# Kernel optimization log

Measured on AMD Instinct MI355X. Metric: run time of the kernel, lower is better.

Reference implementation:

```python
import jax, jax.numpy as jnp
import numpy as np

B, IN, H, CTX = 16384, 1024, 1024, 2048


def setup_inputs() -> dict:
    key = jax.random.key(0)
    ks = jax.random.split(key, 20)
    stdv = 1.0 / np.sqrt(H)
    u = lambda k, shape: jax.random.uniform(k, shape, jnp.float32, -stdv, stdv)
    inp = {
        "y": jax.random.normal(ks[0], (B, IN), jnp.float32),
        "ctx": jax.random.normal(ks[1], (B, CTX), jnp.float32),
        "c0": jax.random.normal(ks[2], (B, H), jnp.float32),
        "h0": jax.random.normal(ks[3], (B, H), jnp.float32),
        # Concatenated gate weights in order (i, f, o, c), matching the
        # per-gate matrices Wi..Wc, Ui..Uc, Ci..Cc of the original module.
        "W": u(ks[4], (4 * H, IN)),   # input projections
        "U": u(ks[5], (4 * H, H)),    # hidden projections
        "C": u(ks[6], (4 * H, CTX)),  # context projections
        "b": u(ks[7], (4 * H,)),      # gate biases
    }
    return inp


def reference(y, ctx, c0, h0, W, U, C, b):
    # One fused GEMM per input stream instead of 12 small ones; same math.
    gates = y @ W.T + h0 @ U.T + ctx @ C.T + b  # [B, 4H]
    gi, gf, go, gc = jnp.split(gates, 4, axis=-1)
    i = jax.nn.sigmoid(gi)
    f = jax.nn.sigmoid(gf)
    o = jax.nn.sigmoid(go)
    c_hat = jnp.tanh(gc)
    c = i * c_hat + f * c0
    h = o * jnp.tanh(c)
    return (c, h)
```

## Files before the change

### kernel.cpp

```cpp
#include <hip/hip_runtime.h>
#include <hip/hip_bf16.h>
#include <stdint.h>

typedef __attribute__((ext_vector_type(8))) short short8;
typedef __attribute__((ext_vector_type(8))) unsigned short ushort8;
typedef __attribute__((ext_vector_type(4))) float f32x4;
typedef __attribute__((ext_vector_type(8))) __bf16 bf16x8;

#define GAS __attribute__((address_space(1)))
#define LAS __attribute__((address_space(3)))

static constexpr int Bn = 16384;
static constexpr int Hn = 1024;
static constexpr int KT = 4096;
static constexpr int BM = 256;
static constexpr int NT = KT / 64;

#define SBAR()   __builtin_amdgcn_s_barrier()
#define VMCNT(n) asm volatile("s_waitcnt vmcnt(" #n ")" ::: "memory")

__device__ __forceinline__ unsigned short f2bf(float f) {
  unsigned u = __builtin_bit_cast(unsigned, f);
  u = (u + 0x7FFFu + ((u >> 16) & 1u)) >> 16;
  return (unsigned short)u;
}

__device__ __forceinline__ float fast_sigm(float x) {
  return __builtin_amdgcn_rcpf(1.f + __expf(-x));
}
__device__ __forceinline__ float fast_tanh(float x) {
  return 1.f - 2.f * __builtin_amdgcn_rcpf(__expf(2.f * x) + 1.f);
}

__global__ __launch_bounds__(256) void cvt_concat_k(
    const float* __restrict__ s0, const float* __restrict__ s1,
    const float* __restrict__ s2, unsigned short* __restrict__ dst,
    long long n8) {
  long long stride = (long long)gridDim.x * blockDim.x;
  for (long long g = (long long)blockIdx.x * blockDim.x + threadIdx.x; g < n8;
       g += stride) {
    long long row = g >> 9;
    int cg = (int)(g & 511) << 3;
    const float* src;
    if (cg < 1024)      src = s0 + row * 1024 + cg;
    else if (cg < 2048) src = s1 + row * 1024 + (cg - 1024);
    else                src = s2 + row * 2048 + (cg - 2048);
    float4 f0 = *(const float4*)src;
    float4 f1 = *(const float4*)(src + 4);
    ushort8 o;
    o[0] = f2bf(f0.x); o[1] = f2bf(f0.y); o[2] = f2bf(f0.z); o[3] = f2bf(f0.w);
    o[4] = f2bf(f1.x); o[5] = f2bf(f1.y); o[6] = f2bf(f1.z); o[7] = f2bf(f1.w);
    *(ushort8*)(dst + (g << 3)) = o;
  }
}

__global__ __launch_bounds__(512, 2) void lstm_gemm(
    const unsigned short* __restrict__ X, const unsigned short* __restrict__ Wc,
    const float* __restrict__ bias, const float* __restrict__ c0,
    float* __restrict__ out_c, float* __restrict__ out_h) {
  extern __shared__ char smem[];

  int bid = blockIdx.x;
  int swz = (bid & 7) * 128 + (bid >> 3);
  int mblk = swz >> 4, cblk = swz & 15;
  int brow0 = mblk * BM;
  int hcol0 = cblk * 64;

  int tid = threadIdx.x;
  int lane = tid & 63, wid = tid >> 6;
  int wr = wid >> 2, wc = wid & 3;

  const char* Xc = (const char*)X;
  const char* Wcc = (const char*)Wc;

  int rr = tid >> 3;
  uint32_t cbyte = (uint32_t)(((tid & 7) * 16) ^ ((rr & 7) << 4));
  uint32_t aoff[2][2], boff[2][2];
#pragma unroll
  for (int half = 0; half < 2; ++half) {
#pragma unroll
    for (int j = 0; j < 2; ++j) {
      int r = half * 128 + j * 64 + rr;
      aoff[half][j] = (uint32_t)(brow0 + r) * (KT * 2) + cbyte;
      int w = ((r >> 4) & 3) * 1024 + hcol0 + ((r >> 6) << 4) + (r & 15);
      boff[half][j] = (uint32_t)w * (KT * 2) + cbyte;
    }
  }

  auto stage_half = [&](int isB, int half, int tt) {
    int ts = tt < NT ? tt : NT - 1;
    int bufs = tt & 1;
#pragma unroll
    for (int j = 0; j < 2; ++j) {
      uint32_t off = (isB ? boff[half][j] : aoff[half][j]) + (uint32_t)ts * 128u;
      const char* src = (isB ? Wcc : Xc) + off;
      char* dst = smem + bufs * 65536 + isB * 32768 + half * 16384 + j * 8192 +
                  wid * 1024;
      __builtin_amdgcn_global_load_lds((const GAS unsigned int*)src,
                                       (LAS unsigned int*)dst, 16, 0, 0);
    }
  };

  int kg = (lane >> 4) << 4;
  int sw = (lane & 7) << 4;
  int koff0 = (0 + kg) ^ sw;
  int koff1 = (64 + kg) ^ sw;
  int fr = lane & 15;

  f32x4 acc[8][4] = {};
  short8 bfr[4][2];

  stage_half(1, 0, 0);
  stage_half(1, 1, 0);
  stage_half(0, 0, 0);
  stage_half(0, 1, 0);
  stage_half(1, 0, 1);
  stage_half(1, 1, 1);
  stage_half(0, 0, 1);
  VMCNT(8);
  SBAR();

  for (int t = 0; t < NT; ++t) {
    int p = t & 1;
#pragma unroll
    for (int q = 0; q < 4; ++q) {
      if (q == 0) {
        int bb = p * 65536 + 32768 + (wc * 64 + fr) * 128;
#pragma unroll
        for (int n = 0; n < 4; ++n) {
          bfr[n][0] = *(const short8*)(smem + bb + n * 2048 + koff0);
          bfr[n][1] = *(const short8*)(smem + bb + n * 2048 + koff1);
        }
      }
      int ab = p * 65536 + ((2 * q + wr) * 32 + fr) * 128;
      short8 a0k0 = *(const short8*)(smem + ab + koff0);
      short8 a0k1 = *(const short8*)(smem + ab + koff1);
      short8 a1k0 = *(const short8*)(smem + ab + 2048 + koff0);
      short8 a1k1 = *(const short8*)(smem + ab + 2048 + koff1);

      if (q == 0)      stage_half(0, 1, t + 1);
      else if (q == 1) stage_half(1, 0, t + 2);
      else if (q == 2) stage_half(1, 1, t + 2);
      else             stage_half(0, 0, t + 2);

      SBAR();
      __builtin_amdgcn_s_setprio(1);
#pragma unroll
      for (int n = 0; n < 4; ++n) {
        acc[2 * q][n] = __builtin_amdgcn_mfma_f32_16x16x32_bf16(
            __builtin_bit_cast(bf16x8, a0k0), __builtin_bit_cast(bf16x8, bfr[n][0]),
            acc[2 * q][n], 0, 0, 0);
        acc[2 * q][n] = __builtin_amdgcn_mfma_f32_16x16x32_bf16(
            __builtin_bit_cast(bf16x8, a0k1), __builtin_bit_cast(bf16x8, bfr[n][1]),
            acc[2 * q][n], 0, 0, 0);
        acc[2 * q + 1][n] = __builtin_amdgcn_mfma_f32_16x16x32_bf16(
            __builtin_bit_cast(bf16x8, a1k0), __builtin_bit_cast(bf16x8, bfr[n][0]),
            acc[2 * q + 1][n], 0, 0, 0);
        acc[2 * q + 1][n] = __builtin_amdgcn_mfma_f32_16x16x32_bf16(
            __builtin_bit_cast(bf16x8, a1k1), __builtin_bit_cast(bf16x8, bfr[n][1]),
            acc[2 * q + 1][n], 0, 0, 0);
      }
      __builtin_amdgcn_s_setprio(0);

      if (q == 1) { VMCNT(10); }
      else if (q == 3) { VMCNT(8); }
      SBAR();
    }
  }

  int col = hcol0 + wc * 16 + fr;
  float bi = bias[col], bf_ = bias[1024 + col];
  float bo = bias[2048 + col], bc = bias[3072 + col];
#pragma unroll
  for (int m = 0; m < 8; ++m) {
    int row0 = brow0 + (2 * (m >> 1) + wr) * 32 + (m & 1) * 16 + ((lane >> 4) << 2);
#pragma unroll
    for (int j = 0; j < 4; ++j) {
      size_t idx = (size_t)(row0 + j) * 1024 + col;
      float i_ = fast_sigm(acc[m][0][j] + bi);
      float f_ = fast_sigm(acc[m][1][j] + bf_);
      float o_ = fast_sigm(acc[m][2][j] + bo);
      float ch = fast_tanh(acc[m][3][j] + bc);
      float cn = i_ * ch + f_ * c0[idx];
      out_c[idx] = cn;
      out_h[idx] = o_ * fast_tanh(cn);
    }
  }
}

__global__ __launch_bounds__(256) void lstm_naive(
    const float* __restrict__ y, const float* __restrict__ ctx,
    const float* __restrict__ c0, const float* __restrict__ h0,
    const float* __restrict__ W, const float* __restrict__ U,
    const float* __restrict__ C, const float* __restrict__ b,
    float* __restrict__ out_c, float* __restrict__ out_h) {
  size_t t = (size_t)blockIdx.x * blockDim.x + threadIdx.x;
  if (t >= (size_t)Bn * Hn) return;
  int row = (int)(t >> 10), col = (int)(t & 1023);
  float g[4];
#pragma unroll
  for (int gg = 0; gg < 4; ++gg) {
    int wrow = gg * 1024 + col;
    float s = b[wrow];
    const float* yr = y + (size_t)row * 1024;
    const float* Wr = W + (size_t)wrow * 1024;
    for (int k = 0; k < 1024; ++k) s += yr[k] * Wr[k];
    const float* hr = h0 + (size_t)row * 1024;
    const float* Ur = U + (size_t)wrow * 1024;
    for (int k = 0; k < 1024; ++k) s += hr[k] * Ur[k];
    const float* cr = ctx + (size_t)row * 2048;
    const float* Cr = C + (size_t)wrow * 2048;
    for (int k = 0; k < 2048; ++k) s += cr[k] * Cr[k];
    g[gg] = s;
  }
  float i_ = fast_sigm(g[0]), f_ = fast_sigm(g[1]);
  float o_ = fast_sigm(g[2]), ch = fast_tanh(g[3]);
  float cn = i_ * ch + f_ * c0[t];
  out_c[t] = cn;
  out_h[t] = o_ * fast_tanh(cn);
}

extern "C" void kernel_launch(void* const* d_in, const int* in_sizes, int n_in,
                              void* d_out, int out_size, void* d_ws, size_t ws_size,
                              hipStream_t stream) {
  const float* y   = (const float*)d_in[0];
  const float* ctx = (const float*)d_in[1];
  const float* c0  = (const float*)d_in[2];
  const float* h0  = (const float*)d_in[3];
  const float* W   = (const float*)d_in[4];
  const float* U   = (const float*)d_in[5];
  const float* C   = (const float*)d_in[6];
  const float* b   = (const float*)d_in[7];
  float* out = (float*)d_out;
  float* out_c = out;
  float* out_h = out + (size_t)Bn * Hn;

  const size_t needX = (size_t)Bn * KT * 2;
  const size_t needW = (size_t)(4 * Hn) * KT * 2;

  if (ws_size >= needX + needW) {
    unsigned short* Xb = (unsigned short*)d_ws;
    unsigned short* Wb = (unsigned short*)((char*)d_ws + needX);
    cvt_concat_k<<<2048, 256, 0, stream>>>(y, h0, ctx, Xb, (long long)Bn * 512);
    cvt_concat_k<<<2048, 256, 0, stream>>>(W, U, C, Wb, (long long)(4 * Hn) * 512);
    (void)hipFuncSetAttribute((const void*)lstm_gemm,
                              hipFuncAttributeMaxDynamicSharedMemorySize, 131072);
    lstm_gemm<<<1024, 512, 131072, stream>>>(Xb, Wb, b, c0, out_c, out_h);
  } else {
    lstm_naive<<<(Bn * Hn + 255) / 256, 256, 0, stream>>>(y, ctx, c0, h0, W, U, C,
                                                          b, out_c, out_h);
  }
}
```

Baseline: 557.2 us.

## Software-pipeline LDS fragment loads one phase ahead of MFMAs

Restructures the main GEMM loop so each phase loads the next phase's A fragments (and, at phase boundaries, the next tile's B k0 fragments) into double-buffered registers before running the current MFMAs. The loop is unrolled by two tiles so buffer indices are compile-time, and the vmcnt waits are moved and retuned. The aim is to hide LDS read latency behind matrix math. In exchange it uses more VGPRs and depends on correct wait and barrier placement for the prefetched buffers.

```diff
diff --git a/kernel.cpp b/kernel.cpp
--- a/kernel.cpp
+++ b/kernel.cpp
@@ -108,7 +108,9 @@
   int fr = lane & 15;
 
   f32x4 acc[8][4] = {};
-  short8 bfr[4][2];
+  short8 areg[2][4];
+  short8 bk0[2][4];
+  short8 bk1[4];
 
   stage_half(1, 0, 0);
   stage_half(1, 1, 0);
@@ -119,54 +121,85 @@
   stage_half(0, 0, 1);
   VMCNT(8);
   SBAR();
-
-  for (int t = 0; t < NT; ++t) {
-    int p = t & 1;
-#pragma unroll
-    for (int q = 0; q < 4; ++q) {
-      if (q == 0) {
-        int bb = p * 65536 + 32768 + (wc * 64 + fr) * 128;
-#pragma unroll
-        for (int n = 0; n < 4; ++n) {
-          bfr[n][0] = *(const short8*)(smem + bb + n * 2048 + koff0);
-          bfr[n][1] = *(const short8*)(smem + bb + n * 2048 + koff1);
-        }
-      }
-      int ab = p * 65536 + ((2 * q + wr) * 32 + fr) * 128;
-      short8 a0k0 = *(const short8*)(smem + ab + koff0);
-      short8 a0k1 = *(const short8*)(smem + ab + koff1);
-      short8 a1k0 = *(const short8*)(smem + ab + 2048 + koff0);
-      short8 a1k1 = *(const short8*)(smem + ab + 2048 + koff1);
-
-      if (q == 0)      stage_half(0, 1, t + 1);
-      else if (q == 1) stage_half(1, 0, t + 2);
-      else if (q == 2) stage_half(1, 1, t + 2);
-      else             stage_half(0, 0, t + 2);
-
-      SBAR();
-      __builtin_amdgcn_s_setprio(1);
-#pragma unroll
-      for (int n = 0; n < 4; ++n) {
-        acc[2 * q][n] = __builtin_amdgcn_mfma_f32_16x16x32_bf16(
-            __builtin_bit_cast(bf16x8, a0k0), __builtin_bit_cast(bf16x8, bfr[n][0]),
-            acc[2 * q][n], 0, 0, 0);
-        acc[2 * q][n] = __builtin_amdgcn_mfma_f32_16x16x32_bf16(
-            __builtin_bit_cast(bf16x8, a0k1), __builtin_bit_cast(bf16x8, bfr[n][1]),
-            acc[2 * q][n], 0, 0, 0);
-        acc[2 * q + 1][n] = __builtin_amdgcn_mfma_f32_16x16x32_bf16(
-            __builtin_bit_cast(bf16x8, a1k0), __builtin_bit_cast(bf16x8, bfr[n][0]),
-            acc[2 * q + 1][n], 0, 0, 0);
-        acc[2 * q + 1][n] = __builtin_amdgcn_mfma_f32_16x16x32_bf16(
-            __builtin_bit_cast(bf16x8, a1k1), __builtin_bit_cast(bf16x8, bfr[n][1]),
-            acc[2 * q + 1][n], 0, 0, 0);
-      }
-      __builtin_amdgcn_s_setprio(0);
-
-      if (q == 1) { VMCNT(10); }
-      else if (q == 3) { VMCNT(8); }
-      SBAR();
-    }
-  }
+  {
+    int bb = 32768 + (wc * 64 + fr) * 128;
+#pragma unroll
+    for (int n = 0; n < 4; ++n)
+      bk0[0][n] = *(const short8*)(smem + bb + n * 2048 + koff0);
+    int ab = (wr * 32 + fr) * 128;
+    areg[0][0] = *(const short8*)(smem + ab + koff0);
+    areg[0][1] = *(const short8*)(smem + ab + koff1);
+    areg[0][2] = *(const short8*)(smem + ab + 2048 + koff0);
+    areg[0][3] = *(const short8*)(smem + ab + 2048 + koff1);
+  }
+
+#define PHASE(Q_, P_, T_)                                                     \
+  {                                                                           \
+    constexpr int Q = (Q_);                                                   \
+    constexpr int P = (P_);                                                   \
+    const int t_ = (T_);                                                      \
+                                                     \
+    if (Q == 0)      stage_half(0, 1, t_ + 1);      \
+    else if (Q == 1) stage_half(1, 0, t_ + 2);      \
+    else if (Q == 2) stage_half(1, 1, t_ + 2);      \
+    else             stage_half(0, 0, t_ + 2);      \
+    if (Q == 0) { VMCNT(8); }                                                 \
+    if (Q == 2) { VMCNT(6); }                                                 \
+                                                \
+    if (Q < 3) {                                                              \
+      int ab = P * 65536 + ((2 * (Q + 1) + wr) * 32 + fr) * 128;              \
+      areg[(Q + 1) & 1][0] = *(const short8*)(smem + ab + koff0);             \
+      areg[(Q + 1) & 1][1] = *(const short8*)(smem + ab + koff1);             \
+      areg[(Q + 1) & 1][2] = *(const short8*)(smem + ab + 2048 + koff0);      \
+      areg[(Q + 1) & 1][3] = *(const short8*)(smem + ab + 2048 + koff1);      \
+    } else {                                                                  \
+      int ab = (P ^ 1) * 65536 + (wr * 32 + fr) * 128;                        \
+      areg[0][0] = *(const short8*)(smem + ab + koff0);                       \
+      areg[0][1] = *(const short8*)(smem + ab + koff1);                       \
+      areg[0][2] = *(const short8*)(smem + ab + 2048 + koff0);                \
+      areg[0][3] = *(const short8*)(smem + ab + 2048 + koff1);                \
+      int bb = (P ^ 1) * 65536 + 32768 + (wc * 64 + fr) * 128;                \
+      _Pragma("unroll")                                                       \
+      for (int n = 0; n < 4; ++n)                                             \
+        bk0[P ^ 1][n] = *(const short8*)(smem + bb + n * 2048 + koff0);       \
+    }                                                                         \
+    if (Q == 0) {                                                             \
+      int bb = P * 65536 + 32768 + (wc * 64 + fr) * 128;                      \
+      _Pragma("unroll")                                                       \
+      for (int n = 0; n < 4; ++n)                                             \
+        bk1[n] = *(const short8*)(smem + bb + n * 2048 + koff1);              \
+    }                                                                         \
+    SBAR();                                                                   \
+    __builtin_amdgcn_s_setprio(1);                                            \
+    _Pragma("unroll")                                                         \
+    for (int n = 0; n < 4; ++n)                                               \
+      acc[2 * Q][n] = __builtin_amdgcn_mfma_f32_16x16x32_bf16(                \
+          __builtin_bit_cast(bf16x8, areg[Q & 1][0]),                         \
+          __builtin_bit_cast(bf16x8, bk0[P][n]), acc[2 * Q][n], 0, 0, 0);     \
+    _Pragma("unroll")                                                         \
+    for (int n = 0; n < 4; ++n)                                               \
+      acc[2 * Q + 1][n] = __builtin_amdgcn_mfma_f32_16x16x32_bf16(            \
+          __builtin_bit_cast(bf16x8, areg[Q & 1][2]),                         \
+          __builtin_bit_cast(bf16x8, bk0[P][n]), acc[2 * Q + 1][n], 0, 0, 0); \
+    _Pragma("unroll")                                                         \
+    for (int n = 0; n < 4; ++n)                                               \
+      acc[2 * Q][n] = __builtin_amdgcn_mfma_f32_16x16x32_bf16(                \
+          __builtin_bit_cast(bf16x8, areg[Q & 1][1]),                         \
+          __builtin_bit_cast(bf16x8, bk1[n]), acc[2 * Q][n], 0, 0, 0);        \
+    _Pragma("unroll")                                                         \
+    for (int n = 0; n < 4; ++n)                                               \
+      acc[2 * Q + 1][n] = __builtin_amdgcn_mfma_f32_16x16x32_bf16(            \
+          __builtin_bit_cast(bf16x8, areg[Q & 1][3]),                         \
+          __builtin_bit_cast(bf16x8, bk1[n]), acc[2 * Q + 1][n], 0, 0, 0);    \
+    __builtin_amdgcn_s_setprio(0);                                            \
+    SBAR();                                                                   \
+  }
+
+  for (int t = 0; t < NT; t += 2) {
+    PHASE(0, 0, t) PHASE(1, 0, t) PHASE(2, 0, t) PHASE(3, 0, t)
+    PHASE(0, 1, t + 1) PHASE(1, 1, t + 1) PHASE(2, 1, t + 1) PHASE(3, 1, t + 1)
+  }
+#undef PHASE
 
   int col = hcol0 + wc * 16 + fr;
   float bi = bias[col], bf_ = bias[1024 + col];
```

After: 566.5 us. No clear change (+1.7%).

## Restructure GEMM main loop into two-phase pipeline with register-prefetched A fragments

Applied to the files above, without the earlier changes.

Replaces the four-quarter inner loop with two phases per K-tile. The A fragments for the next tile's first half are loaded into registers while the second half computes, and staging of the following tiles is reordered around that. Block-to-tile mapping also changes so consecutive blocks walk the M dimension instead of the column blocks. The goal is fewer barriers per K step and more overlap of LDS reads with MFMA work, at the cost of higher register pressure and a more fragile vmcnt/stage ordering.

```diff
diff --git a/kernel.cpp b/kernel.cpp
--- a/kernel.cpp
+++ b/kernel.cpp
@@ -62,7 +62,7 @@
 
   int bid = blockIdx.x;
   int swz = (bid & 7) * 128 + (bid >> 3);
-  int mblk = swz >> 4, cblk = swz & 15;
+  int mblk = swz & 63, cblk = swz >> 6;
   int brow0 = mblk * BM;
   int hcol0 = cblk * 64;
 
@@ -108,65 +108,107 @@
   int fr = lane & 15;
 
   f32x4 acc[8][4] = {};
-  short8 bfr[4][2];
-
+  short8 areg0[8];
+  short8 areg1[8];
+  short8 bk0[4], bk1[4];
+
+  stage_half(0, 0, 0);
+  stage_half(0, 1, 0);
   stage_half(1, 0, 0);
   stage_half(1, 1, 0);
-  stage_half(0, 0, 0);
-  stage_half(0, 1, 0);
-  stage_half(1, 0, 1);
-  stage_half(1, 1, 1);
   stage_half(0, 0, 1);
-  VMCNT(8);
+  VMCNT(2);
   SBAR();
+  {
+#pragma unroll
+    for (int qq = 0; qq < 2; ++qq) {
+      int ab = ((2 * qq + wr) * 32 + fr) * 128;
+      areg0[qq * 4 + 0] = *(const short8*)(smem + ab + koff0);
+      areg0[qq * 4 + 1] = *(const short8*)(smem + ab + koff1);
+      areg0[qq * 4 + 2] = *(const short8*)(smem + ab + 2048 + koff0);
+      areg0[qq * 4 + 3] = *(const short8*)(smem + ab + 2048 + koff1);
+    }
+  }
+
+#define MFMA16(ACCB, AR)                                                      \
+  _Pragma("unroll")                                                           \
+  for (int qq = 0; qq < 2; ++qq) {                                            \
+    _Pragma("unroll")                                                         \
+    for (int n = 0; n < 4; ++n) {                                             \
+      acc[(ACCB) + 2 * qq][n] = __builtin_amdgcn_mfma_f32_16x16x32_bf16(      \
+          __builtin_bit_cast(bf16x8, AR[qq * 4 + 0]),                         \
+          __builtin_bit_cast(bf16x8, bk0[n]), acc[(ACCB) + 2 * qq][n], 0, 0,  \
+          0);                                                                 \
+      acc[(ACCB) + 2 * qq + 1][n] = __builtin_amdgcn_mfma_f32_16x16x32_bf16(  \
+          __builtin_bit_cast(bf16x8, AR[qq * 4 + 2]),                         \
+          __builtin_bit_cast(bf16x8, bk0[n]), acc[(ACCB) + 2 * qq + 1][n], 0, \
+          0, 0);                                                              \
+    }                                                                         \
+  }                                                                           \
+  _Pragma("unroll")                                                           \
+  for (int qq = 0; qq < 2; ++qq) {                                            \
+    _Pragma("unroll")                                                         \
+    for (int n = 0; n < 4; ++n) {                                             \
+      acc[(ACCB) + 2 * qq][n] = __builtin_amdgcn_mfma_f32_16x16x32_bf16(      \
+          __builtin_bit_cast(bf16x8, AR[qq * 4 + 1]),                         \
+          __builtin_bit_cast(bf16x8, bk1[n]), acc[(ACCB) + 2 * qq][n], 0, 0,  \
+          0);                                                                 \
+      acc[(ACCB) + 2 * qq + 1][n] = __builtin_amdgcn_mfma_f32_16x16x32_bf16(  \
+          __builtin_bit_cast(bf16x8, AR[qq * 4 + 3]),                         \
+          __builtin_bit_cast(bf16x8, bk1[n]), acc[(ACCB) + 2 * qq + 1][n], 0, \
+          0, 0);                                                              \
+    }                                                                         \
+  }
 
   for (int t = 0; t < NT; ++t) {
     int p = t & 1;
-#pragma unroll
-    for (int q = 0; q < 4; ++q) {
-      if (q == 0) {
-        int bb = p * 65536 + 32768 + (wc * 64 + fr) * 128;
-#pragma unroll
-        for (int n = 0; n < 4; ++n) {
-          bfr[n][0] = *(const short8*)(smem + bb + n * 2048 + koff0);
-          bfr[n][1] = *(const short8*)(smem + bb + n * 2048 + koff1);
-        }
+    int pb = p * 65536;
+    stage_half(0, 1, t + 1);
+    stage_half(1, 0, t + 1);
+    stage_half(1, 1, t + 1);
+    {
+      int bb = pb + 32768 + (wc * 64 + fr) * 128;
+#pragma unroll
+      for (int n = 0; n < 4; ++n) {
+        bk0[n] = *(const short8*)(smem + bb + n * 2048 + koff0);
+        bk1[n] = *(const short8*)(smem + bb + n * 2048 + koff1);
       }
-      int ab = p * 65536 + ((2 * q + wr) * 32 + fr) * 128;
-      short8 a0k0 = *(const short8*)(smem + ab + koff0);
-      short8 a0k1 = *(const short8*)(smem + ab + koff1);
-      short8 a1k0 = *(const short8*)(smem + ab + 2048 + koff0);
-      short8 a1k1 = *(const short8*)(smem + ab + 2048 + koff1);
-
-      if (q == 0)      stage_half(0, 1, t + 1);
-      else if (q == 1) stage_half(1, 0, t + 2);
-      else if (q == 2) stage_half(1, 1, t + 2);
-      else             stage_half(0, 0, t + 2);
-
-      SBAR();
-      __builtin_amdgcn_s_setprio(1);
-#pragma unroll
-      for (int n = 0; n < 4; ++n) {
-        acc[2 * q][n] = __builtin_amdgcn_mfma_f32_16x16x32_bf16(
-            __builtin_bit_cast(bf16x8, a0k0), __builtin_bit_cast(bf16x8, bfr[n][0]),
-            acc[2 * q][n], 0, 0, 0);
-        acc[2 * q][n] = __builtin_amdgcn_mfma_f32_16x16x32_bf16(
-            __builtin_bit_cast(bf16x8, a0k1), __builtin_bit_cast(bf16x8, bfr[n][1]),
-            acc[2 * q][n], 0, 0, 0);
-        acc[2 * q + 1][n] = __builtin_amdgcn_mfma_f32_16x16x32_bf16(
-            __builtin_bit_cast(bf16x8, a1k0), __builtin_bit_cast(bf16x8, bfr[n][0]),
-            acc[2 * q + 1][n], 0, 0, 0);
-        acc[2 * q + 1][n] = __builtin_amdgcn_mfma_f32_16x16x32_bf16(
-            __builtin_bit_cast(bf16x8, a1k1), __builtin_bit_cast(bf16x8, bfr[n][1]),
-            acc[2 * q + 1][n], 0, 0, 0);
+    }
+    {
+#pragma unroll
+      for (int qq = 0; qq < 2; ++qq) {
+        int ab = pb + ((2 * (qq + 2) + wr) * 32 + fr) * 128;
+        areg1[qq * 4 + 0] = *(const short8*)(smem + ab + koff0);
+        areg1[qq * 4 + 1] = *(const short8*)(smem + ab + koff1);
+        areg1[qq * 4 + 2] = *(const short8*)(smem + ab + 2048 + koff0);
+        areg1[qq * 4 + 3] = *(const short8*)(smem + ab + 2048 + koff1);
       }
-      __builtin_amdgcn_s_setprio(0);
-
-      if (q == 1) { VMCNT(10); }
-      else if (q == 3) { VMCNT(8); }
-      SBAR();
-    }
-  }
+    }
+    SBAR();
+    __builtin_amdgcn_s_setprio(1);
+    MFMA16(0, areg0)
+    __builtin_amdgcn_s_setprio(0);
+    VMCNT(6);
+    SBAR();
+    stage_half(0, 0, t + 2);
+    {
+#pragma unroll
+      for (int qq = 0; qq < 2; ++qq) {
+        int ab = (pb ^ 65536) + ((2 * qq + wr) * 32 + fr) * 128;
+        areg0[qq * 4 + 0] = *(const short8*)(smem + ab + koff0);
+        areg0[qq * 4 + 1] = *(const short8*)(smem + ab + koff1);
+        areg0[qq * 4 + 2] = *(const short8*)(smem + ab + 2048 + koff0);
+        areg0[qq * 4 + 3] = *(const short8*)(smem + ab + 2048 + koff1);
+      }
+    }
+    SBAR();
+    __builtin_amdgcn_s_setprio(1);
+    MFMA16(4, areg1)
+    __builtin_amdgcn_s_setprio(0);
+    VMCNT(2);
+    SBAR();
+  }
+#undef MFMA16
 
   int col = hcol0 + wc * 16 + fr;
   float bi = bias[col], bf_ = bias[1024 + col];
```

Result: slower. 587.4 us (+5.4%).

## Switch GEMM to 32x32x16 MFMA with 4x2 wave tiling and reworked pipeline

Applied to the files above, without the earlier changes.

Replaces the 16x16x32 bf16 MFMA inner loop with 32x32x16 MFMAs and reassigns the 8 waves to a 4x2 grid, so each wave covers 64 rows by 128 gate columns. The weight row mapping is changed to match. The LDS load and global_load_lds staging schedule is restructured into a single loop body with interleaved A/B fragment loads and barriers. The aim is fewer LDS reads per MFMA and higher MFMA throughput; the cost is larger accumulator register pressure and a tighter prefetch/wait schedule that may stall.

```diff
diff --git a/kernel.cpp b/kernel.cpp
--- a/kernel.cpp
+++ b/kernel.cpp
@@ -4,7 +4,7 @@
 
 typedef __attribute__((ext_vector_type(8))) short short8;
 typedef __attribute__((ext_vector_type(8))) unsigned short ushort8;
-typedef __attribute__((ext_vector_type(4))) float f32x4;
+typedef __attribute__((ext_vector_type(16))) float f32x16;
 typedef __attribute__((ext_vector_type(8))) __bf16 bf16x8;
 
 #define GAS __attribute__((address_space(1)))
@@ -13,7 +13,6 @@
 static constexpr int Bn = 16384;
 static constexpr int Hn = 1024;
 static constexpr int KT = 4096;
-static constexpr int BM = 256;
 static constexpr int NT = KT / 64;
 
 #define SBAR()   __builtin_amdgcn_s_barrier()
@@ -63,12 +62,12 @@
   int bid = blockIdx.x;
   int swz = (bid & 7) * 128 + (bid >> 3);
   int mblk = swz >> 4, cblk = swz & 15;
-  int brow0 = mblk * BM;
+  int brow0 = mblk * 256;
   int hcol0 = cblk * 64;
 
   int tid = threadIdx.x;
   int lane = tid & 63, wid = tid >> 6;
-  int wr = wid >> 2, wc = wid & 3;
+  int wr = wid >> 1, wc = wid & 1;
 
   const char* Xc = (const char*)X;
   const char* Wcc = (const char*)Wc;
@@ -82,7 +81,7 @@
     for (int j = 0; j < 2; ++j) {
       int r = half * 128 + j * 64 + rr;
       aoff[half][j] = (uint32_t)(brow0 + r) * (KT * 2) + cbyte;
-      int w = ((r >> 4) & 3) * 1024 + hcol0 + ((r >> 6) << 4) + (r & 15);
+      int w = ((r >> 5) & 3) * 1024 + hcol0 + ((r >> 7) << 5) + (r & 31);
       boff[half][j] = (uint32_t)w * (KT * 2) + cbyte;
     }
   }
@@ -101,86 +100,110 @@
     }
   };
 
-  int kg = (lane >> 4) << 4;
+  int l31 = lane & 31;
   int sw = (lane & 7) << 4;
-  int koff0 = (0 + kg) ^ sw;
-  int koff1 = (64 + kg) ^ sw;
-  int fr = lane & 15;
-
-  f32x4 acc[8][4] = {};
-  short8 bfr[4][2];
-
+  int kb = (lane >> 5) << 4;
+  int k_[4];
+#pragma unroll
+  for (int ks = 0; ks < 4; ++ks) k_[ks] = (ks * 32 + kb) ^ sw;
+  uint32_t abase = (uint32_t)(wr * 64 + l31) * 128;
+  uint32_t bbase = 32768u + (uint32_t)(wc * 128 + l31) * 128;
+
+#define LDA(PB, RF, KOFF) \
+  *(const short8*)(smem + (PB) + abase + (RF) * 4096 + (KOFF))
+#define LDB(PB, CF, KOFF) \
+  *(const short8*)(smem + (PB) + bbase + (CF) * 4096 + (KOFF))
+
+  f32x16 acc[2][4] = {};
+  short8 areg[2][2];
+  short8 bfr[4][4];
+
+  stage_half(0, 0, 0);
+  stage_half(0, 1, 0);
   stage_half(1, 0, 0);
   stage_half(1, 1, 0);
-  stage_half(0, 0, 0);
-  stage_half(0, 1, 0);
   stage_half(1, 0, 1);
-  stage_half(1, 1, 1);
-  stage_half(0, 0, 1);
-  VMCNT(8);
+  VMCNT(2);
   SBAR();
+  {
+#pragma unroll
+    for (int cf = 0; cf < 4; ++cf) {
+      bfr[cf][0] = LDB(0, cf, k_[0]);
+      bfr[cf][1] = LDB(0, cf, k_[1]);
+    }
+    areg[0][0] = LDA(0, 0, k_[0]);
+    areg[0][1] = LDA(0, 0, k_[1]);
+  }
+
+#define MFMA8(RF, KH, PAR)                                                    \
+  __builtin_amdgcn_s_setprio(1);                                              \
+  _Pragma("unroll")                                                           \
+  for (int cf = 0; cf < 4; ++cf)                                              \
+    acc[RF][cf] = __builtin_amdgcn_mfma_f32_32x32x16_bf16(                    \
+        __builtin_bit_cast(bf16x8, areg[PAR][0]),                             \
+        __builtin_bit_cast(bf16x8, bfr[cf][2 * (KH)]), acc[RF][cf], 0, 0, 0); \
+  _Pragma("unroll")                                                           \
+  for (int cf = 0; cf < 4; ++cf)                                              \
+    acc[RF][cf] = __builtin_amdgcn_mfma_f32_32x32x16_bf16(                    \
+        __builtin_bit_cast(bf16x8, areg[PAR][1]),                             \
+        __builtin_bit_cast(bf16x8, bfr[cf][2 * (KH) + 1]), acc[RF][cf], 0, 0, \
+        0);                                                                   \
+  __builtin_amdgcn_s_setprio(0);
 
   for (int t = 0; t < NT; ++t) {
-    int p = t & 1;
-#pragma unroll
-    for (int q = 0; q < 4; ++q) {
-      if (q == 0) {
-        int bb = p * 65536 + 32768 + (wc * 64 + fr) * 128;
-#pragma unroll
-        for (int n = 0; n < 4; ++n) {
-          bfr[n][0] = *(const short8*)(smem + bb + n * 2048 + koff0);
-          bfr[n][1] = *(const short8*)(smem + bb + n * 2048 + koff1);
-        }
-      }
-      int ab = p * 65536 + ((2 * q + wr) * 32 + fr) * 128;
-      short8 a0k0 = *(const short8*)(smem + ab + koff0);
-      short8 a0k1 = *(const short8*)(smem + ab + koff1);
-      short8 a1k0 = *(const short8*)(smem + ab + 2048 + koff0);
-      short8 a1k1 = *(const short8*)(smem + ab + 2048 + koff1);
-
-      if (q == 0)      stage_half(0, 1, t + 1);
-      else if (q == 1) stage_half(1, 0, t + 2);
-      else if (q == 2) stage_half(1, 1, t + 2);
-      else             stage_half(0, 0, t + 2);
-
-      SBAR();
-      __builtin_amdgcn_s_setprio(1);
-#pragma unroll
-      for (int n = 0; n < 4; ++n) {
-        acc[2 * q][n] = __builtin_amdgcn_mfma_f32_16x16x32_bf16(
-            __builtin_bit_cast(bf16x8, a0k0), __builtin_bit_cast(bf16x8, bfr[n][0]),
-            acc[2 * q][n], 0, 0, 0);
-        acc[2 * q][n] = __builtin_amdgcn_mfma_f32_16x16x32_bf16(
-            __builtin_bit_cast(bf16x8, a0k1), __builtin_bit_cast(bf16x8, bfr[n][1]),
-            acc[2 * q][n], 0, 0, 0);
-        acc[2 * q + 1][n] = __builtin_amdgcn_mfma_f32_16x16x32_bf16(
-            __builtin_bit_cast(bf16x8, a1k0), __builtin_bit_cast(bf16x8, bfr[n][0]),
-            acc[2 * q + 1][n], 0, 0, 0);
-        acc[2 * q + 1][n] = __builtin_amdgcn_mfma_f32_16x16x32_bf16(
-            __builtin_bit_cast(bf16x8, a1k1), __builtin_bit_cast(bf16x8, bfr[n][1]),
-            acc[2 * q + 1][n], 0, 0, 0);
-      }
-      __builtin_amdgcn_s_setprio(0);
-
-      if (q == 1) { VMCNT(10); }
-      else if (q == 3) { VMCNT(8); }
-      SBAR();
-    }
-  }
-
-  int col = hcol0 + wc * 16 + fr;
+    int pb = (t & 1) * 65536;
+    int qb = pb ^ 65536;
+    stage_half(0, 0, t + 1);
+    stage_half(0, 1, t + 1);
+    stage_half(1, 1, t + 1);
+    areg[1][0] = LDA(pb, 1, k_[0]);
+    areg[1][1] = LDA(pb, 1, k_[1]);
+    MFMA8(0, 0, 0)
+    SBAR();
+    areg[0][0] = LDA(pb, 0, k_[2]);
+    areg[0][1] = LDA(pb, 0, k_[3]);
+#pragma unroll
+    for (int cf = 0; cf < 4; ++cf) {
+      bfr[cf][2] = LDB(pb, cf, k_[2]);
+      bfr[cf][3] = LDB(pb, cf, k_[3]);
+    }
+    MFMA8(1, 0, 1)
+    SBAR();
+    areg[1][0] = LDA(pb, 1, k_[2]);
+    areg[1][1] = LDA(pb, 1, k_[3]);
+    MFMA8(0, 1, 0)
+    SBAR();
+    stage_half(1, 0, t + 2);
+    VMCNT(2);
+    SBAR();
+#pragma unroll
+    for (int cf = 0; cf < 4; ++cf) {
+      bfr[cf][0] = LDB(qb, cf, k_[0]);
+      bfr[cf][1] = LDB(qb, cf, k_[1]);
+    }
+    areg[0][0] = LDA(qb, 0, k_[0]);
+    areg[0][1] = LDA(qb, 0, k_[1]);
+    MFMA8(1, 1, 1)
+    SBAR();
+  }
+#undef MFMA8
+#undef LDA
+#undef LDB
+
+  int col = hcol0 + wc * 32 + l31;
   float bi = bias[col], bf_ = bias[1024 + col];
   float bo = bias[2048 + col], bc = bias[3072 + col];
 #pragma unroll
-  for (int m = 0; m < 8; ++m) {
-    int row0 = brow0 + (2 * (m >> 1) + wr) * 32 + (m & 1) * 16 + ((lane >> 4) << 2);
-#pragma unroll
-    for (int j = 0; j < 4; ++j) {
-      size_t idx = (size_t)(row0 + j) * 1024 + col;
-      float i_ = fast_sigm(acc[m][0][j] + bi);
-      float f_ = fast_sigm(acc[m][1][j] + bf_);
-      float o_ = fast_sigm(acc[m][2][j] + bo);
-      float ch = fast_tanh(acc[m][3][j] + bc);
+  for (int rf = 0; rf < 2; ++rf) {
+    int rbase = brow0 + wr * 64 + rf * 32 + ((lane >> 5) << 2);
+#pragma unroll
+    for (int reg = 0; reg < 16; ++reg) {
+      int grow = rbase + (reg & 3) + ((reg >> 2) << 3);
+      size_t idx = (size_t)grow * 1024 + col;
+      float i_ = fast_sigm(acc[rf][0][reg] + bi);
+      float f_ = fast_sigm(acc[rf][1][reg] + bf_);
+      float o_ = fast_sigm(acc[rf][2][reg] + bo);
+      float ch = fast_tanh(acc[rf][3][reg] + bc);
       float cn = i_ * ch + f_ * c0[idx];
       out_c[idx] = cn;
       out_h[idx] = o_ * fast_tanh(cn);
```

Result: slower. 618.8 us (+11.1%).
